# Performance work log

Hardware: AMD Instinct MI355X
Metric: run time of the kernel (lower is better)

## Reference

```python
import math
import jax, jax.numpy as jnp
import numpy as np

B = 65536
EMBED = 256
COND = 256
TIME = 128
HID = 256
E = 8
RHID = 128
IN_DIM = EMBED + TIME + COND  # 640


def setup_inputs() -> dict:
    key = jax.random.key(0)
    ks = jax.random.split(key, 20)
    s = 0.02
    inp = {
        "z_t": jax.random.normal(ks[0], (B, EMBED), jnp.float32),
        "t": jax.random.uniform(ks[1], (B, 1), jnp.float32),
        "cond": jax.random.normal(ks[2], (B, COND), jnp.float32),
        # time embedding proj (Linear(time,time) -> SiLU -> Linear(time,time))
        "tW1": jax.random.normal(ks[3], (TIME, TIME), jnp.float32) * s,
        "tb1": jnp.zeros((TIME,), jnp.float32),
        "tW2": jax.random.normal(ks[4], (TIME, TIME), jnp.float32) * s,
        "tb2": jnp.zeros((TIME,), jnp.float32),
        # stacked expert weights [E, in, out]
        "eW1": jax.random.normal(ks[5], (E, IN_DIM, HID), jnp.float32) * s,
        "eb1": jnp.zeros((E, HID), jnp.float32),
        "eW2": jax.random.normal(ks[6], (E, HID, HID), jnp.float32) * s,
        "eb2": jnp.zeros((E, HID), jnp.float32),
        "eW3": jax.random.normal(ks[7], (E, HID, EMBED), jnp.float32) * s,
        "eb3": jnp.zeros((E, EMBED), jnp.float32),
        # router
        "rW1": jax.random.normal(ks[8], (IN_DIM, RHID), jnp.float32) * s,
        "rb1": jnp.zeros((RHID,), jnp.float32),
        "rW2": jax.random.normal(ks[9], (RHID, E), jnp.float32) * s,
        "rb2": jnp.zeros((E,), jnp.float32),
    }
    return inp


def _time_embedding(t, tW1, tb1, tW2, tb2):
    half = TIME // 2  # 64
    scale = -math.log(10000.0) / (half - 1)
    freqs = jnp.exp(jnp.arange(half, dtype=t.dtype) * scale)[None, :]  # [1, half]
    angles = t * freqs  # [B, half]
    emb = jnp.concatenate([jnp.sin(angles), jnp.cos(angles)], axis=-1)  # [B, TIME]
    h = jax.nn.silu(emb @ tW1 + tb1)
    return h @ tW2 + tb2


def reference(z_t, t, cond, tW1, tb1, tW2, tb2, eW1, eb1, eW2, eb2, eW3, eb3, rW1, rb1, rW2, rb2):
    time_emb = _time_embedding(t, tW1, tb1, tW2, tb2)
    x = jnp.concatenate([z_t, time_emb, cond], axis=-1)  # [B, IN_DIM]
    # dense MoE: all experts via batched GEMMs (dropout=0 -> identity)
    h1 = jax.nn.silu(jnp.einsum('bi,eih->beh', x, eW1) + eb1)      # [B,E,HID]
    h2 = jax.nn.silu(jnp.einsum('beh,ehk->bek', h1, eW2) + eb2)    # [B,E,HID]
    expert_out = jnp.einsum('beh,ehd->bed', h2, eW3) + eb3         # [B,E,EMBED]
    # router softmax gate
    rh = jax.nn.silu(x @ rW1 + rb1)
    gate = jax.nn.softmax(rh @ rW2 + rb2, axis=-1)                 # [B,E]
    velocity = jnp.einsum('be,bed->bd', gate, expert_out)          # [B,EMBED]
    return velocity, gate
```

## Files before the change

### kernel.cpp

```cpp
#include <hip/hip_runtime.h>

typedef __attribute__((ext_vector_type(8))) short bf16x8;
typedef __attribute__((ext_vector_type(4))) float f32x4;

#define NB_ROWS 65536
#define D_EMBED 256
#define D_HID   256
#define N_EXP   8
#define D_RHID  128
#define D_IN    640

#define KSTR 72
#define HSTR 264

static __device__ __forceinline__ ushort f2bf(float f) {
  union { float f; unsigned u; } v; v.f = f;
  unsigned r = v.u + 0x7fffu + ((v.u >> 16) & 1u);
  return (ushort)(r >> 16);
}
static __device__ __forceinline__ float bf2f(ushort h) {
  union { unsigned u; float f; } v; v.u = ((unsigned)h) << 16;
  return v.f;
}
static __device__ __forceinline__ float silu_f(float x) {
  return x / (1.0f + __expf(-x));
}

__global__ void prep_transpose(const float* __restrict__ src, ushort* __restrict__ dst,
                               int R, int C, int total) {
  int idx = blockIdx.x * 256 + threadIdx.x;
  if (idx >= total) return;
  int rc = R * C;
  int m = idx / rc;
  int rem = idx - m * rc;
  int r = rem / C;
  int c = rem - r * C;
  dst[m * rc + c * R + r] = f2bf(src[idx]);
}

static __device__ __forceinline__ void stageA128_512(const ushort* __restrict__ src, int ld,
                                                     int kt, ushort* dst, int tid) {
  uint4 v[2];
  #pragma unroll
  for (int c = 0; c < 2; ++c) {
    int f = c * 8192 + tid * 16;
    int r = f >> 7, ce = (f & 127) >> 1;
    v[c] = *(const uint4*)&src[(size_t)r * ld + kt + ce];
  }
  #pragma unroll
  for (int c = 0; c < 2; ++c) {
    int f = c * 8192 + tid * 16;
    int r = f >> 7, ce = (f & 127) >> 1;
    *(uint4*)&dst[r * KSTR + ce] = v[c];
  }
}
static __device__ __forceinline__ void stageB256_512(const ushort* __restrict__ src, int ld,
                                                     int kt, ushort* dst, int tid) {
  uint4 v[4];
  #pragma unroll
  for (int c = 0; c < 4; ++c) {
    int f = c * 8192 + tid * 16;
    int r = f >> 7, ce = (f & 127) >> 1;
    v[c] = *(const uint4*)&src[(size_t)r * ld + kt + ce];
  }
  #pragma unroll
  for (int c = 0; c < 4; ++c) {
    int f = c * 8192 + tid * 16;
    int r = f >> 7, ce = (f & 127) >> 1;
    *(uint4*)&dst[r * KSTR + ce] = v[c];
  }
}
static __device__ __forceinline__ void stageA128_256(const ushort* __restrict__ src, int ld,
                                                     int kt, ushort* dst, int tid) {
  uint4 v[4];
  #pragma unroll
  for (int c = 0; c < 4; ++c) {
    int f = c * 4096 + tid * 16;
    int r = f >> 7, ce = (f & 127) >> 1;
    v[c] = *(const uint4*)&src[(size_t)r * ld + kt + ce];
  }
  #pragma unroll
  for (int c = 0; c < 4; ++c) {
    int f = c * 4096 + tid * 16;
    int r = f >> 7, ce = (f & 127) >> 1;
    *(uint4*)&dst[r * KSTR + ce] = v[c];
  }
}

__global__ __launch_bounds__(512) void time_x_kernel(
    const float* __restrict__ zt, const float* __restrict__ tin,
    const float* __restrict__ cond,
    const ushort* __restrict__ tw1t, const ushort* __restrict__ tw2t,
    const float* __restrict__ tb1, const float* __restrict__ tb2,
    ushort* __restrict__ x) {
  __shared__ __align__(16) ushort sE[128 * 136];
  __shared__ float sFreq[64];
  __shared__ float sB1[128];
  __shared__ float sB2[128];

  const int tid = threadIdx.x;
  const int row0 = blockIdx.x * 128;

  for (int ch = tid; ch < 128 * 64; ch += 512) {
    int r = ch >> 6;
    int c4 = (ch & 63) << 2;
    size_t grow = (size_t)(row0 + r);
    float4 zv = *(const float4*)&zt[grow * 256 + c4];
    ushort4 o; o.x = f2bf(zv.x); o.y = f2bf(zv.y); o.z = f2bf(zv.z); o.w = f2bf(zv.w);
    *(ushort4*)&x[grow * 640 + c4] = o;
    float4 cv = *(const float4*)&cond[grow * 256 + c4];
    ushort4 o2; o2.x = f2bf(cv.x); o2.y = f2bf(cv.y); o2.z = f2bf(cv.z); o2.w = f2bf(cv.w);
    *(ushort4*)&x[grow * 640 + 384 + c4] = o2;
  }

  if (tid < 64) sFreq[tid] = __expf((float)tid * (-9.210340371976184f / 63.0f));
  if (tid < 128) { sB1[tid] = tb1[tid]; sB2[tid] = tb2[tid]; }
  __syncthreads();

  {
    int r = tid >> 2;
    int qd = tid & 3;
    float tv = tin[row0 + r];
    int half = qd >> 1;
    int cbase = (qd & 1) * 32;
    ushort* er = &sE[r * 136 + half * 64 + cbase];
    #pragma unroll
    for (int c = 0; c < 32; ++c) {
      float a = tv * sFreq[cbase + c];
      float v = half ? __cosf(a) : __sinf(a);
      er[c] = f2bf(v);
    }
  }
  __syncthreads();

  const int l = tid & 63;
  const int w = tid >> 6;
  const int wm = w >> 1;
  const int wn = w & 1;
  const int lr = l & 15;
  const int lk = (l >> 4) * 8;
  const int q4 = (l >> 4) * 4;

  f32x4 acc[2][4] = {};
  #pragma unroll
  for (int kk = 0; kk < 4; ++kk) {
    int kb = kk * 32 + lk;
    bf16x8 av[2], bv[4];
    #pragma unroll
    for (int mf = 0; mf < 2; ++mf)
      av[mf] = *(const bf16x8*)&sE[(wm * 32 + mf * 16 + lr) * 136 + kb];
    #pragma unroll
    for (int nf = 0; nf < 4; ++nf)
      bv[nf] = *(const bf16x8*)&tw1t[(size_t)(wn * 64 + nf * 16 + lr) * 128 + kb];
    #pragma unroll
    for (int mf = 0; mf < 2; ++mf)
      #pragma unroll
      for (int nf = 0; nf < 4; ++nf)
        acc[mf][nf] = __builtin_amdgcn_mfma_f32_16x16x32_bf16(av[mf], bv[nf], acc[mf][nf], 0, 0, 0);
  }
  __syncthreads();
  #pragma unroll
  for (int mf = 0; mf < 2; ++mf)
    #pragma unroll
    for (int nf = 0; nf < 4; ++nf) {
      int cc = wn * 64 + nf * 16 + lr;
      #pragma unroll
      for (int rg = 0; rg < 4; ++rg) {
        int rr = wm * 32 + mf * 16 + q4 + rg;
        sE[rr * 136 + cc] = f2bf(silu_f(acc[mf][nf][rg] + sB1[cc]));
      }
    }
  __syncthreads();

  f32x4 acc2[2][4] = {};
  #pragma unroll
  for (int kk = 0; kk < 4; ++kk) {
    int kb = kk * 32 + lk;
    bf16x8 av[2], bv[4];
    #pragma unroll
    for (int mf = 0; mf < 2; ++mf)
      av[mf] = *(const bf16x8*)&sE[(wm * 32 + mf * 16 + lr) * 136 + kb];
    #pragma unroll
    for (int nf = 0; nf < 4; ++nf)
      bv[nf] = *(const bf16x8*)&tw2t[(size_t)(wn * 64 + nf * 16 + lr) * 128 + kb];
    #pragma unroll
    for (int mf = 0; mf < 2; ++mf)
      #pragma unroll
      for (int nf = 0; nf < 4; ++nf)
        acc2[mf][nf] = __builtin_amdgcn_mfma_f32_16x16x32_bf16(av[mf], bv[nf], acc2[mf][nf], 0, 0, 0);
  }
  #pragma unroll
  for (int mf = 0; mf < 2; ++mf)
    #pragma unroll
    for (int nf = 0; nf < 4; ++nf) {
      int cc = wn * 64 + nf * 16 + lr;
      #pragma unroll
      for (int rg = 0; rg < 4; ++rg) {
        int rr = wm * 32 + mf * 16 + q4 + rg;
        x[(size_t)(row0 + rr) * 640 + 256 + cc] = f2bf(acc2[mf][nf][rg] + sB2[cc]);
      }
    }
}

__global__ __launch_bounds__(256) void router_kernel(
    const ushort* __restrict__ xb, const ushort* __restrict__ rw1t,
    const float* __restrict__ rb1, const float* __restrict__ rW2,
    const float* __restrict__ rb2, float* __restrict__ gatef,
    float* __restrict__ gateo) {
  __shared__ __align__(16) ushort smA[128 * KSTR];
  __shared__ __align__(16) ushort smB[128 * KSTR];
  __shared__ __align__(16) ushort rhbuf[128 * 136];
  __shared__ float sW2[128 * 8];

  const int tid = threadIdx.x;
  const int row0 = blockIdx.x * 128;
  for (int i = tid; i < 1024; i += 256) sW2[i] = rW2[i];

  const int l = tid & 63;
  const int w = tid >> 6;
  const int wm = w >> 1, wn = w & 1;
  const int lr = l & 15, lk = (l >> 4) * 8, q4 = (l >> 4) * 4;
  const ushort* xrow = xb + (size_t)row0 * 640;

  f32x4 acc[4][4] = {};
  for (int kt = 0; kt < 640; kt += 64) {
    stageA128_256(xrow, 640, kt, smA, tid);
    stageA128_256(rw1t, 640, kt, smB, tid);
    __syncthreads();
    #pragma unroll
    for (int kk = 0; kk < 2; ++kk) {
      int kb = kk * 32 + lk;
      bf16x8 av[4], bv[4];
      #pragma unroll
      for (int mf = 0; mf < 4; ++mf)
        av[mf] = *(const bf16x8*)&smA[(wm * 64 + mf * 16 + lr) * KSTR + kb];
      #pragma unroll
      for (int nf = 0; nf < 4; ++nf)
        bv[nf] = *(const bf16x8*)&smB[(wn * 64 + nf * 16 + lr) * KSTR + kb];
      #pragma unroll
      for (int mf = 0; mf < 4; ++mf)
        #pragma unroll
        for (int nf = 0; nf < 4; ++nf)
          acc[mf][nf] = __builtin_amdgcn_mfma_f32_16x16x32_bf16(av[mf], bv[nf], acc[mf][nf], 0, 0, 0);
    }
    __syncthreads();
  }
  #pragma unroll
  for (int nf = 0; nf < 4; ++nf) {
    int cc = wn * 64 + nf * 16 + lr;
    float b1v = rb1[cc];
    #pragma unroll
    for (int mf = 0; mf < 4; ++mf)
      #pragma unroll
      for (int rg = 0; rg < 4; ++rg) {
        int rr = wm * 64 + mf * 16 + q4 + rg;
        rhbuf[rr * 136 + cc] = f2bf(silu_f(acc[mf][nf][rg] + b1v));
      }
  }
  __syncthreads();

  if (tid < 128) {
    float a[8];
    #pragma unroll
    for (int e = 0; e < 8; ++e) a[e] = rb2[e];
    #pragma unroll
    for (int i8 = 0; i8 < 16; ++i8) {
      bf16x8 hv = *(const bf16x8*)&rhbuf[tid * 136 + i8 * 8];
      #pragma unroll
      for (int j = 0; j < 8; ++j) {
        float h = bf2f((ushort)hv[j]);
        const float* wrow = &sW2[(i8 * 8 + j) * 8];
        #pragma unroll
        for (int e = 0; e < 8; ++e) a[e] += h * wrow[e];
      }
    }
    float mx = a[0];
    #pragma unroll
    for (int e = 1; e < 8; ++e) mx = fmaxf(mx, a[e]);
    float s = 0.f, ex[8];
    #pragma unroll
    for (int e = 0; e < 8; ++e) { ex[e] = __expf(a[e] - mx); s += ex[e]; }
    float inv = 1.f / s;
    size_t b = (size_t)(row0 + tid);
    #pragma unroll
    for (int e = 0; e < 8; ++e) {
      float g = ex[e] * inv;
      gatef[b * 8 + e] = g;
      gateo[b * 8 + e] = g;
    }
  }
}

__global__ __launch_bounds__(512) void moe_fused_kernel(
    const ushort* __restrict__ xb, const ushort* __restrict__ w1t,
    const ushort* __restrict__ w2t, const ushort* __restrict__ w3t,
    const float* __restrict__ eb1, const float* __restrict__ eb2,
    const float* __restrict__ eb3, const float* __restrict__ gatef,
    float* __restrict__ velout) {
  __shared__ __align__(16) ushort smA[128 * KSTR];
  __shared__ __align__(16) ushort smB[256 * KSTR];
  __shared__ __align__(16) ushort hbuf[128 * HSTR];
  __shared__ float sGate[128 * 8];
  __shared__ float sEb3[8 * 256];

  const int tid = threadIdx.x;
  const int row0 = blockIdx.x * 128;
  const int l = tid & 63;
  const int w = tid >> 6;
  const int wm = w >> 2;
  const int wn = w & 3;
  const int lr = l & 15;
  const int lk = (l >> 4) * 8;
  const int q4 = (l >> 4) * 4;

  for (int i = tid; i < 1024; i += 512) sGate[i] = gatef[(size_t)row0 * 8 + i];
  for (int i = tid; i < 2048; i += 512) sEb3[i] = eb3[i];

  const ushort* xrow = xb + (size_t)row0 * 640;
  f32x4 vacc[4][4] = {};
  __syncthreads();

  for (int e = 0; e < 8; ++e) {
    const ushort* W1 = w1t + (size_t)e * (256 * 640);
    const ushort* W2 = w2t + (size_t)e * (256 * 256);
    const ushort* W3 = w3t + (size_t)e * (256 * 256);

    f32x4 acc[4][4] = {};
    for (int kt = 0; kt < 640; kt += 64) {
      stageA128_512(xrow, 640, kt, smA, tid);
      stageB256_512(W1, 640, kt, smB, tid);
      __syncthreads();
      #pragma unroll
      for (int kk = 0; kk < 2; ++kk) {
        int kb = kk * 32 + lk;
        bf16x8 av[4], bv[4];
        #pragma unroll
        for (int mf = 0; mf < 4; ++mf)
          av[mf] = *(const bf16x8*)&smA[(wm * 64 + mf * 16 + lr) * KSTR + kb];
        #pragma unroll
        for (int nf = 0; nf < 4; ++nf)
          bv[nf] = *(const bf16x8*)&smB[(wn * 64 + nf * 16 + lr) * KSTR + kb];
        #pragma unroll
        for (int mf = 0; mf < 4; ++mf)
          #pragma unroll
          for (int nf = 0; nf < 4; ++nf)
            acc[mf][nf] = __builtin_amdgcn_mfma_f32_16x16x32_bf16(av[mf], bv[nf], acc[mf][nf], 0, 0, 0);
      }
      __syncthreads();
    }
    #pragma unroll
    for (int nf = 0; nf < 4; ++nf) {
      int cc = wn * 64 + nf * 16 + lr;
      float b1v = eb1[e * 256 + cc];
      #pragma unroll
      for (int mf = 0; mf < 4; ++mf)
        #pragma unroll
        for (int rg = 0; rg < 4; ++rg) {
          int rr = wm * 64 + mf * 16 + q4 + rg;
          hbuf[rr * HSTR + cc] = f2bf(silu_f(acc[mf][nf][rg] + b1v));
        }
    }
    __syncthreads();

    #pragma unroll
    for (int mf = 0; mf < 4; ++mf)
      #pragma unroll
      for (int nf = 0; nf < 4; ++nf)
        acc[mf][nf] = (f32x4){0.f, 0.f, 0.f, 0.f};
    for (int kt = 0; kt < 256; kt += 64) {
      stageB256_512(W2, 256, kt, smB, tid);
      __syncthreads();
      #pragma unroll
      for (int kk = 0; kk < 2; ++kk) {
        int kbl = kk * 32 + lk;
        int kbh = kt + kbl;
        bf16x8 av[4], bv[4];
        #pragma unroll
        for (int mf = 0; mf < 4; ++mf)
          av[mf] = *(const bf16x8*)&hbuf[(wm * 64 + mf * 16 + lr) * HSTR + kbh];
        #pragma unroll
        for (int nf = 0; nf < 4; ++nf)
          bv[nf] = *(const bf16x8*)&smB[(wn * 64 + nf * 16 + lr) * KSTR + kbl];
        #pragma unroll
        for (int mf = 0; mf < 4; ++mf)
          #pragma unroll
          for (int nf = 0; nf < 4; ++nf)
            acc[mf][nf] = __builtin_amdgcn_mfma_f32_16x16x32_bf16(av[mf], bv[nf], acc[mf][nf], 0, 0, 0);
      }
      __syncthreads();
    }
    #pragma unroll
    for (int nf = 0; nf < 4; ++nf) {
      int cc = wn * 64 + nf * 16 + lr;
      float b2v = eb2[e * 256 + cc];
      #pragma unroll
      for (int mf = 0; mf < 4; ++mf)
        #pragma unroll
        for (int rg = 0; rg < 4; ++rg) {
          int rr = wm * 64 + mf * 16 + q4 + rg;
          float gv = sGate[rr * 8 + e];
          hbuf[rr * HSTR + cc] = f2bf(silu_f(acc[mf][nf][rg] + b2v) * gv);
        }
    }
    __syncthreads();

    for (int kt = 0; kt < 256; kt += 64) {
      stageB256_512(W3, 256, kt, smB, tid);
      __syncthreads();
      #pragma unroll
      for (int kk = 0; kk < 2; ++kk) {
        int kbl = kk * 32 + lk;
        int kbh = kt + kbl;
        bf16x8 av[4], bv[4];
        #pragma unroll
        for (int mf = 0; mf < 4; ++mf)
          av[mf] = *(const bf16x8*)&hbuf[(wm * 64 + mf * 16 + lr) * HSTR + kbh];
        #pragma unroll
        for (int nf = 0; nf < 4; ++nf)
          bv[nf] = *(const bf16x8*)&smB[(wn * 64 + nf * 16 + lr) * KSTR + kbl];
        #pragma unroll
        for (int mf = 0; mf < 4; ++mf)
          #pragma unroll
          for (int nf = 0; nf < 4; ++nf)
            vacc[mf][nf] = __builtin_amdgcn_mfma_f32_16x16x32_bf16(av[mf], bv[nf], vacc[mf][nf], 0, 0, 0);
      }
      __syncthreads();
    }
  }

  #pragma unroll
  for (int mf = 0; mf < 4; ++mf)
    #pragma unroll
    for (int rg = 0; rg < 4; ++rg) {
      int rr = wm * 64 + mf * 16 + q4 + rg;
      const float* gp = &sGate[rr * 8];
      #pragma unroll
      for (int nf = 0; nf < 4; ++nf) {
        int cc = wn * 64 + nf * 16 + lr;
        float bsum = 0.f;
        #pragma unroll
        for (int ee = 0; ee < 8; ++ee) bsum += gp[ee] * sEb3[ee * 256 + cc];
        velout[(size_t)(row0 + rr) * D_EMBED + cc] = vacc[mf][nf][rg] + bsum;
      }
    }
}

extern "C" void kernel_launch(void* const* d_in, const int* in_sizes, int n_in,
                              void* d_out, int out_size, void* d_ws, size_t ws_size,
                              hipStream_t stream) {
  const float* zt   = (const float*)d_in[0];
  const float* tin  = (const float*)d_in[1];
  const float* cond = (const float*)d_in[2];
  const float* tW1  = (const float*)d_in[3];
  const float* tb1  = (const float*)d_in[4];
  const float* tW2  = (const float*)d_in[5];
  const float* tb2  = (const float*)d_in[6];
  const float* eW1  = (const float*)d_in[7];
  const float* eb1  = (const float*)d_in[8];
  const float* eW2  = (const float*)d_in[9];
  const float* eb2  = (const float*)d_in[10];
  const float* eW3  = (const float*)d_in[11];
  const float* eb3  = (const float*)d_in[12];
  const float* rW1  = (const float*)d_in[13];
  const float* rb1  = (const float*)d_in[14];
  const float* rW2  = (const float*)d_in[15];
  const float* rb2  = (const float*)d_in[16];

  char* wp = (char*)d_ws;
  ushort* xb    = (ushort*)wp; wp += (size_t)NB_ROWS * D_IN * 2;
  float*  gatef = (float*)wp;  wp += (size_t)NB_ROWS * 8 * 4;
  ushort* w1t   = (ushort*)wp; wp += (size_t)N_EXP * D_HID * D_IN * 2;
  ushort* w2t   = (ushort*)wp; wp += (size_t)N_EXP * D_HID * D_HID * 2;
  ushort* w3t   = (ushort*)wp; wp += (size_t)N_EXP * D_HID * D_EMBED * 2;
  ushort* rw1t  = (ushort*)wp; wp += (size_t)D_RHID * D_IN * 2;
  ushort* tw1t  = (ushort*)wp; wp += (size_t)128 * 128 * 2;
  ushort* tw2t  = (ushort*)wp; wp += (size_t)128 * 128 * 2;

  float* velout  = (float*)d_out;
  float* gateout = velout + (size_t)NB_ROWS * D_EMBED;

  {
    int tot;
    tot = 128 * 128;
    prep_transpose<<<(tot + 255) / 256, 256, 0, stream>>>(tW1, tw1t, 128, 128, tot);
    prep_transpose<<<(tot + 255) / 256, 256, 0, stream>>>(tW2, tw2t, 128, 128, tot);
    tot = D_IN * D_RHID;
    prep_transpose<<<(tot + 255) / 256, 256, 0, stream>>>(rW1, rw1t, D_IN, D_RHID, tot);
    tot = N_EXP * D_IN * D_HID;
    prep_transpose<<<(tot + 255) / 256, 256, 0, stream>>>(eW1, w1t, D_IN, D_HID, tot);
    tot = N_EXP * D_HID * D_HID;
    prep_transpose<<<(tot + 255) / 256, 256, 0, stream>>>(eW2, w2t, D_HID, D_HID, tot);
    tot = N_EXP * D_HID * D_EMBED;
    prep_transpose<<<(tot + 255) / 256, 256, 0, stream>>>(eW3, w3t, D_HID, D_EMBED, tot);
  }

  time_x_kernel<<<512, 512, 0, stream>>>(zt, tin, cond, tw1t, tw2t, tb1, tb2, xb);
  router_kernel<<<512, 256, 0, stream>>>(xb, rw1t, rb1, rW2, rb2, gatef, gateout);
  moe_fused_kernel<<<512, 512, 0, stream>>>(xb, w1t, w2t, w3t, eb1, eb2, eb3, gatef, velout);
}
```

Baseline: 694.2 us.

## Prefetch next K-tile into registers while computing current tile in expert GEMMs

Splits the shared-memory staging helpers into separate global-load and LDS-write steps, so the next K-slice of activations and weights is loaded into registers before the MFMA work on the current slice begins. All three expert GEMM loops now issue their global loads early, which hides load latency behind matrix work. The cost is more live registers, which could lower occupancy in an already register-heavy kernel, and each iteration now has two barriers.

```diff
diff --git a/kernel.cpp b/kernel.cpp
--- a/kernel.cpp
+++ b/kernel.cpp
@@ -38,15 +38,16 @@
   dst[m * rc + c * R + r] = f2bf(src[idx]);
 }
 
-static __device__ __forceinline__ void stageA128_512(const ushort* __restrict__ src, int ld,
-                                                     int kt, ushort* dst, int tid) {
-  uint4 v[2];
+static __device__ __forceinline__ void loadA128_512(const ushort* __restrict__ src, int ld,
+                                                    int kt, int tid, uint4* v) {
   #pragma unroll
   for (int c = 0; c < 2; ++c) {
     int f = c * 8192 + tid * 16;
     int r = f >> 7, ce = (f & 127) >> 1;
     v[c] = *(const uint4*)&src[(size_t)r * ld + kt + ce];
   }
+}
+static __device__ __forceinline__ void writeA128_512(ushort* dst, int tid, const uint4* v) {
   #pragma unroll
   for (int c = 0; c < 2; ++c) {
     int f = c * 8192 + tid * 16;
@@ -54,15 +55,16 @@
     *(uint4*)&dst[r * KSTR + ce] = v[c];
   }
 }
-static __device__ __forceinline__ void stageB256_512(const ushort* __restrict__ src, int ld,
-                                                     int kt, ushort* dst, int tid) {
-  uint4 v[4];
+static __device__ __forceinline__ void loadB256_512(const ushort* __restrict__ src, int ld,
+                                                    int kt, int tid, uint4* v) {
   #pragma unroll
   for (int c = 0; c < 4; ++c) {
     int f = c * 8192 + tid * 16;
     int r = f >> 7, ce = (f & 127) >> 1;
     v[c] = *(const uint4*)&src[(size_t)r * ld + kt + ce];
   }
+}
+static __device__ __forceinline__ void writeB256_512(ushort* dst, int tid, const uint4* v) {
   #pragma unroll
   for (int c = 0; c < 4; ++c) {
     int f = c * 8192 + tid * 16;
@@ -326,27 +328,43 @@
     const ushort* W3 = w3t + (size_t)e * (256 * 256);
 
     f32x4 acc[4][4] = {};
-    for (int kt = 0; kt < 640; kt += 64) {
-      stageA128_512(xrow, 640, kt, smA, tid);
-      stageB256_512(W1, 640, kt, smB, tid);
+    {
+      uint4 va[2], vb[4];
+      loadA128_512(xrow, 640, 0, tid, va);
+      loadB256_512(W1, 640, 0, tid, vb);
+      writeA128_512(smA, tid, va);
+      writeB256_512(smB, tid, vb);
       __syncthreads();
-      #pragma unroll
-      for (int kk = 0; kk < 2; ++kk) {
-        int kb = kk * 32 + lk;
-        bf16x8 av[4], bv[4];
-        #pragma unroll
-        for (int mf = 0; mf < 4; ++mf)
-          av[mf] = *(const bf16x8*)&smA[(wm * 64 + mf * 16 + lr) * KSTR + kb];
-        #pragma unroll
-        for (int nf = 0; nf < 4; ++nf)
-          bv[nf] = *(const bf16x8*)&smB[(wn * 64 + nf * 16 + lr) * KSTR + kb];
-        #pragma unroll
-        for (int mf = 0; mf < 4; ++mf)
+      for (int kt = 0; kt < 640; kt += 64) {
+        const bool more = (kt + 64 < 640);
+        uint4 na[2], nb[4];
+        if (more) {
+          loadA128_512(xrow, 640, kt + 64, tid, na);
+          loadB256_512(W1, 640, kt + 64, tid, nb);
+        }
+        #pragma unroll
+        for (int kk = 0; kk < 2; ++kk) {
+          int kb = kk * 32 + lk;
+          bf16x8 av[4], bv[4];
+          #pragma unroll
+          for (int mf = 0; mf < 4; ++mf)
+            av[mf] = *(const bf16x8*)&smA[(wm * 64 + mf * 16 + lr) * KSTR + kb];
           #pragma unroll
           for (int nf = 0; nf < 4; ++nf)
-            acc[mf][nf] = __builtin_amdgcn_mfma_f32_16x16x32_bf16(av[mf], bv[nf], acc[mf][nf], 0, 0, 0);
-      }
-      __syncthreads();
+            bv[nf] = *(const bf16x8*)&smB[(wn * 64 + nf * 16 + lr) * KSTR + kb];
+          #pragma unroll
+          for (int mf = 0; mf < 4; ++mf)
+            #pragma unroll
+            for (int nf = 0; nf < 4; ++nf)
+              acc[mf][nf] = __builtin_amdgcn_mfma_f32_16x16x32_bf16(av[mf], bv[nf], acc[mf][nf], 0, 0, 0);
+        }
+        __syncthreads();
+        if (more) {
+          writeA128_512(smA, tid, na);
+          writeB256_512(smB, tid, nb);
+        }
+        __syncthreads();
+      }
     }
     #pragma unroll
     for (int nf = 0; nf < 4; ++nf) {
@@ -367,27 +385,36 @@
       #pragma unroll
       for (int nf = 0; nf < 4; ++nf)
         acc[mf][nf] = (f32x4){0.f, 0.f, 0.f, 0.f};
-    for (int kt = 0; kt < 256; kt += 64) {
-      stageB256_512(W2, 256, kt, smB, tid);
+    {
+      uint4 vb[4];
+      loadB256_512(W2, 256, 0, tid, vb);
+      writeB256_512(smB, tid, vb);
       __syncthreads();
-      #pragma unroll
-      for (int kk = 0; kk < 2; ++kk) {
-        int kbl = kk * 32 + lk;
-        int kbh = kt + kbl;
-        bf16x8 av[4], bv[4];
-        #pragma unroll
-        for (int mf = 0; mf < 4; ++mf)
-          av[mf] = *(const bf16x8*)&hbuf[(wm * 64 + mf * 16 + lr) * HSTR + kbh];
-        #pragma unroll
-        for (int nf = 0; nf < 4; ++nf)
-          bv[nf] = *(const bf16x8*)&smB[(wn * 64 + nf * 16 + lr) * KSTR + kbl];
-        #pragma unroll
-        for (int mf = 0; mf < 4; ++mf)
+      for (int kt = 0; kt < 256; kt += 64) {
+        const bool more = (kt + 64 < 256);
+        uint4 nb[4];
+        if (more) loadB256_512(W2, 256, kt + 64, tid, nb);
+        #pragma unroll
+        for (int kk = 0; kk < 2; ++kk) {
+          int kbl = kk * 32 + lk;
+          int kbh = kt + kbl;
+          bf16x8 av[4], bv[4];
+          #pragma unroll
+          for (int mf = 0; mf < 4; ++mf)
+            av[mf] = *(const bf16x8*)&hbuf[(wm * 64 + mf * 16 + lr) * HSTR + kbh];
           #pragma unroll
           for (int nf = 0; nf < 4; ++nf)
-            acc[mf][nf] = __builtin_amdgcn_mfma_f32_16x16x32_bf16(av[mf], bv[nf], acc[mf][nf], 0, 0, 0);
-      }
-      __syncthreads();
+            bv[nf] = *(const bf16x8*)&smB[(wn * 64 + nf * 16 + lr) * KSTR + kbl];
+          #pragma unroll
+          for (int mf = 0; mf < 4; ++mf)
+            #pragma unroll
+            for (int nf = 0; nf < 4; ++nf)
+              acc[mf][nf] = __builtin_amdgcn_mfma_f32_16x16x32_bf16(av[mf], bv[nf], acc[mf][nf], 0, 0, 0);
+        }
+        __syncthreads();
+        if (more) writeB256_512(smB, tid, nb);
+        __syncthreads();
+      }
     }
     #pragma unroll
     for (int nf = 0; nf < 4; ++nf) {
@@ -404,27 +431,36 @@
     }
     __syncthreads();
 
-    for (int kt = 0; kt < 256; kt += 64) {
-      stageB256_512(W3, 256, kt, smB, tid);
+    {
+      uint4 vb[4];
+      loadB256_512(W3, 256, 0, tid, vb);
+      writeB256_512(smB, tid, vb);
       __syncthreads();
-      #pragma unroll
-      for (int kk = 0; kk < 2; ++kk) {
-        int kbl = kk * 32 + lk;
-        int kbh = kt + kbl;
-        bf16x8 av[4], bv[4];
-        #pragma unroll
-        for (int mf = 0; mf < 4; ++mf)
-          av[mf] = *(const bf16x8*)&hbuf[(wm * 64 + mf * 16 + lr) * HSTR + kbh];
-        #pragma unroll
-        for (int nf = 0; nf < 4; ++nf)
-          bv[nf] = *(const bf16x8*)&smB[(wn * 64 + nf * 16 + lr) * KSTR + kbl];
-        #pragma unroll
-        for (int mf = 0; mf < 4; ++mf)
+      for (int kt = 0; kt < 256; kt += 64) {
+        const bool more = (kt + 64 < 256);
+        uint4 nb[4];
+        if (more) loadB256_512(W3, 256, kt + 64, tid, nb);
+        #pragma unroll
+        for (int kk = 0; kk < 2; ++kk) {
+          int kbl = kk * 32 + lk;
+          int kbh = kt + kbl;
+          bf16x8 av[4], bv[4];
+          #pragma unroll
+          for (int mf = 0; mf < 4; ++mf)
+            av[mf] = *(const bf16x8*)&hbuf[(wm * 64 + mf * 16 + lr) * HSTR + kbh];
           #pragma unroll
           for (int nf = 0; nf < 4; ++nf)
-            vacc[mf][nf] = __builtin_amdgcn_mfma_f32_16x16x32_bf16(av[mf], bv[nf], vacc[mf][nf], 0, 0, 0);
-      }
-      __syncthreads();
+            bv[nf] = *(const bf16x8*)&smB[(wn * 64 + nf * 16 + lr) * KSTR + kbl];
+          #pragma unroll
+          for (int mf = 0; mf < 4; ++mf)
+            #pragma unroll
+            for (int nf = 0; nf < 4; ++nf)
+              vacc[mf][nf] = __builtin_amdgcn_mfma_f32_16x16x32_bf16(av[mf], bv[nf], vacc[mf][nf], 0, 0, 0);
+        }
+        __syncthreads();
+        if (more) writeB256_512(smB, tid, nb);
+        __syncthreads();
+      }
     }
   }
 
```

After: 1.032 ms. +48.7%, slower.

## Halve MoE row tile, swizzle hidden buffer, and double grid for occupancy

Applied to the files above, without the earlier changes.

The fused MoE kernel now handles 64 rows per block instead of 128 and launches 1024 blocks. Per-wave accumulators shrink to 2x4 fragments and the launch bounds ask for several resident blocks. The padded hidden buffer becomes an XOR-swizzled 64x256 layout to avoid LDS bank conflicts without padding. The expert-3 bias table is loaded into the reused A-staging buffer only at the end, so LDS drops enough for more blocks per CU, giving better latency hiding. In exchange, expert weight tiles are re-staged twice as often per row, and the tighter register budget risks spills.

```diff
diff --git a/kernel.cpp b/kernel.cpp
--- a/kernel.cpp
+++ b/kernel.cpp
@@ -11,7 +11,6 @@
 #define D_IN    640
 
 #define KSTR 72
-#define HSTR 264
 
 static __device__ __forceinline__ ushort f2bf(float f) {
   union { float f; unsigned u; } v; v.f = f;
@@ -24,6 +23,10 @@
 }
 static __device__ __forceinline__ float silu_f(float x) {
   return x / (1.0f + __expf(-x));
+}
+
+static __device__ __forceinline__ int hswz(int r, int c) {
+  return r * 256 + ((((c) >> 3) ^ (r & 7)) << 3) + ((c) & 7);
 }
 
 __global__ void prep_transpose(const float* __restrict__ src, ushort* __restrict__ dst,
@@ -38,21 +41,12 @@
   dst[m * rc + c * R + r] = f2bf(src[idx]);
 }
 
-static __device__ __forceinline__ void stageA128_512(const ushort* __restrict__ src, int ld,
-                                                     int kt, ushort* dst, int tid) {
-  uint4 v[2];
-  #pragma unroll
-  for (int c = 0; c < 2; ++c) {
-    int f = c * 8192 + tid * 16;
-    int r = f >> 7, ce = (f & 127) >> 1;
-    v[c] = *(const uint4*)&src[(size_t)r * ld + kt + ce];
-  }
-  #pragma unroll
-  for (int c = 0; c < 2; ++c) {
-    int f = c * 8192 + tid * 16;
-    int r = f >> 7, ce = (f & 127) >> 1;
-    *(uint4*)&dst[r * KSTR + ce] = v[c];
-  }
+static __device__ __forceinline__ void stageA64_512(const ushort* __restrict__ src, int ld,
+                                                    int kt, ushort* dst, int tid) {
+  int f = tid * 16;
+  int r = f >> 7, ce = (f & 127) >> 1;
+  uint4 v = *(const uint4*)&src[(size_t)r * ld + kt + ce];
+  *(uint4*)&dst[r * KSTR + ce] = v;
 }
 static __device__ __forceinline__ void stageB256_512(const ushort* __restrict__ src, int ld,
                                                      int kt, ushort* dst, int tid) {
@@ -291,20 +285,19 @@
   }
 }
 
-__global__ __launch_bounds__(512) void moe_fused_kernel(
+__global__ __launch_bounds__(512, 4) void moe_fused_kernel(
     const ushort* __restrict__ xb, const ushort* __restrict__ w1t,
     const ushort* __restrict__ w2t, const ushort* __restrict__ w3t,
     const float* __restrict__ eb1, const float* __restrict__ eb2,
     const float* __restrict__ eb3, const float* __restrict__ gatef,
     float* __restrict__ velout) {
-  __shared__ __align__(16) ushort smA[128 * KSTR];
+  __shared__ __align__(16) ushort smA[64 * KSTR];
   __shared__ __align__(16) ushort smB[256 * KSTR];
-  __shared__ __align__(16) ushort hbuf[128 * HSTR];
-  __shared__ float sGate[128 * 8];
-  __shared__ float sEb3[8 * 256];
+  __shared__ __align__(16) ushort hbuf[64 * 256];
+  __shared__ float sGate[64 * 8];
 
   const int tid = threadIdx.x;
-  const int row0 = blockIdx.x * 128;
+  const int row0 = blockIdx.x * 64;
   const int l = tid & 63;
   const int w = tid >> 6;
   const int wm = w >> 2;
@@ -313,11 +306,10 @@
   const int lk = (l >> 4) * 8;
   const int q4 = (l >> 4) * 4;
 
-  for (int i = tid; i < 1024; i += 512) sGate[i] = gatef[(size_t)row0 * 8 + i];
-  for (int i = tid; i < 2048; i += 512) sEb3[i] = eb3[i];
+  for (int i = tid; i < 512; i += 512) sGate[i] = gatef[(size_t)row0 * 8 + i];
 
   const ushort* xrow = xb + (size_t)row0 * 640;
-  f32x4 vacc[4][4] = {};
+  f32x4 vacc[2][4] = {};
   __syncthreads();
 
   for (int e = 0; e < 8; ++e) {
@@ -325,23 +317,23 @@
     const ushort* W2 = w2t + (size_t)e * (256 * 256);
     const ushort* W3 = w3t + (size_t)e * (256 * 256);
 
-    f32x4 acc[4][4] = {};
+    f32x4 acc[2][4] = {};
     for (int kt = 0; kt < 640; kt += 64) {
-      stageA128_512(xrow, 640, kt, smA, tid);
+      stageA64_512(xrow, 640, kt, smA, tid);
       stageB256_512(W1, 640, kt, smB, tid);
       __syncthreads();
       #pragma unroll
       for (int kk = 0; kk < 2; ++kk) {
         int kb = kk * 32 + lk;
-        bf16x8 av[4], bv[4];
-        #pragma unroll
-        for (int mf = 0; mf < 4; ++mf)
-          av[mf] = *(const bf16x8*)&smA[(wm * 64 + mf * 16 + lr) * KSTR + kb];
+        bf16x8 av[2], bv[4];
+        #pragma unroll
+        for (int mf = 0; mf < 2; ++mf)
+          av[mf] = *(const bf16x8*)&smA[(wm * 32 + mf * 16 + lr) * KSTR + kb];
         #pragma unroll
         for (int nf = 0; nf < 4; ++nf)
           bv[nf] = *(const bf16x8*)&smB[(wn * 64 + nf * 16 + lr) * KSTR + kb];
         #pragma unroll
-        for (int mf = 0; mf < 4; ++mf)
+        for (int mf = 0; mf < 2; ++mf)
           #pragma unroll
           for (int nf = 0; nf < 4; ++nf)
             acc[mf][nf] = __builtin_amdgcn_mfma_f32_16x16x32_bf16(av[mf], bv[nf], acc[mf][nf], 0, 0, 0);
@@ -353,17 +345,17 @@
       int cc = wn * 64 + nf * 16 + lr;
       float b1v = eb1[e * 256 + cc];
       #pragma unroll
-      for (int mf = 0; mf < 4; ++mf)
+      for (int mf = 0; mf < 2; ++mf)
         #pragma unroll
         for (int rg = 0; rg < 4; ++rg) {
-          int rr = wm * 64 + mf * 16 + q4 + rg;
-          hbuf[rr * HSTR + cc] = f2bf(silu_f(acc[mf][nf][rg] + b1v));
+          int rr = wm * 32 + mf * 16 + q4 + rg;
+          hbuf[hswz(rr, cc)] = f2bf(silu_f(acc[mf][nf][rg] + b1v));
         }
     }
     __syncthreads();
 
     #pragma unroll
-    for (int mf = 0; mf < 4; ++mf)
+    for (int mf = 0; mf < 2; ++mf)
       #pragma unroll
       for (int nf = 0; nf < 4; ++nf)
         acc[mf][nf] = (f32x4){0.f, 0.f, 0.f, 0.f};
@@ -374,15 +366,15 @@
       for (int kk = 0; kk < 2; ++kk) {
         int kbl = kk * 32 + lk;
         int kbh = kt + kbl;
-        bf16x8 av[4], bv[4];
-        #pragma unroll
-        for (int mf = 0; mf < 4; ++mf)
-          av[mf] = *(const bf16x8*)&hbuf[(wm * 64 + mf * 16 + lr) * HSTR + kbh];
+        bf16x8 av[2], bv[4];
+        #pragma unroll
+        for (int mf = 0; mf < 2; ++mf)
+          av[mf] = *(const bf16x8*)&hbuf[hswz(wm * 32 + mf * 16 + lr, kbh)];
         #pragma unroll
         for (int nf = 0; nf < 4; ++nf)
           bv[nf] = *(const bf16x8*)&smB[(wn * 64 + nf * 16 + lr) * KSTR + kbl];
         #pragma unroll
-        for (int mf = 0; mf < 4; ++mf)
+        for (int mf = 0; mf < 2; ++mf)
           #pragma unroll
           for (int nf = 0; nf < 4; ++nf)
             acc[mf][nf] = __builtin_amdgcn_mfma_f32_16x16x32_bf16(av[mf], bv[nf], acc[mf][nf], 0, 0, 0);
@@ -394,12 +386,12 @@
       int cc = wn * 64 + nf * 16 + lr;
       float b2v = eb2[e * 256 + cc];
       #pragma unroll
-      for (int mf = 0; mf < 4; ++mf)
+      for (int mf = 0; mf < 2; ++mf)
         #pragma unroll
         for (int rg = 0; rg < 4; ++rg) {
-          int rr = wm * 64 + mf * 16 + q4 + rg;
+          int rr = wm * 32 + mf * 16 + q4 + rg;
           float gv = sGate[rr * 8 + e];
-          hbuf[rr * HSTR + cc] = f2bf(silu_f(acc[mf][nf][rg] + b2v) * gv);
+          hbuf[hswz(rr, cc)] = f2bf(silu_f(acc[mf][nf][rg] + b2v) * gv);
         }
     }
     __syncthreads();
@@ -411,15 +403,15 @@
       for (int kk = 0; kk < 2; ++kk) {
         int kbl = kk * 32 + lk;
         int kbh = kt + kbl;
-        bf16x8 av[4], bv[4];
-        #pragma unroll
-        for (int mf = 0; mf < 4; ++mf)
-          av[mf] = *(const bf16x8*)&hbuf[(wm * 64 + mf * 16 + lr) * HSTR + kbh];
+        bf16x8 av[2], bv[4];
+        #pragma unroll
+        for (int mf = 0; mf < 2; ++mf)
+          av[mf] = *(const bf16x8*)&hbuf[hswz(wm * 32 + mf * 16 + lr, kbh)];
         #pragma unroll
         for (int nf = 0; nf < 4; ++nf)
           bv[nf] = *(const bf16x8*)&smB[(wn * 64 + nf * 16 + lr) * KSTR + kbl];
         #pragma unroll
-        for (int mf = 0; mf < 4; ++mf)
+        for (int mf = 0; mf < 2; ++mf)
           #pragma unroll
           for (int nf = 0; nf < 4; ++nf)
             vacc[mf][nf] = __builtin_amdgcn_mfma_f32_16x16x32_bf16(av[mf], bv[nf], vacc[mf][nf], 0, 0, 0);
@@ -428,18 +420,21 @@
     }
   }
 
-  #pragma unroll
-  for (int mf = 0; mf < 4; ++mf)
+  float* eL = (float*)smA;
+  for (int i = tid; i < 2048; i += 512) eL[i] = eb3[i];
+  __syncthreads();
+  #pragma unroll
+  for (int mf = 0; mf < 2; ++mf)
     #pragma unroll
     for (int rg = 0; rg < 4; ++rg) {
-      int rr = wm * 64 + mf * 16 + q4 + rg;
+      int rr = wm * 32 + mf * 16 + q4 + rg;
       const float* gp = &sGate[rr * 8];
       #pragma unroll
       for (int nf = 0; nf < 4; ++nf) {
         int cc = wn * 64 + nf * 16 + lr;
         float bsum = 0.f;
         #pragma unroll
-        for (int ee = 0; ee < 8; ++ee) bsum += gp[ee] * sEb3[ee * 256 + cc];
+        for (int ee = 0; ee < 8; ++ee) bsum += gp[ee] * eL[ee * 256 + cc];
         velout[(size_t)(row0 + rr) * D_EMBED + cc] = vacc[mf][nf][rg] + bsum;
       }
     }
@@ -496,5 +491,5 @@
 
   time_x_kernel<<<512, 512, 0, stream>>>(zt, tin, cond, tw1t, tw2t, tb1, tb2, xb);
   router_kernel<<<512, 256, 0, stream>>>(xb, rw1t, rb1, rW2, rb2, gatef, gateout);
-  moe_fused_kernel<<<512, 512, 0, stream>>>(xb, w1t, w2t, w3t, eb1, eb2, eb3, gatef, velout);
-}
+  moe_fused_kernel<<<1024, 512, 0, stream>>>(xb, w1t, w2t, w3t, eb1, eb2, eb3, gatef, velout);
+}
```

New measurement: 1.100 ms. 58.4% more time.

## Stream expert weights from global directly into MFMA, keep x tile resident

Applied to the files above, without the earlier changes.

The fused MoE kernel now loads the block's 64x640 input tile into LDS once, and each wave reads its slice of the expert weight columns straight from global/L2 into registers for MFMA. This removes per-k-tile weight staging through LDS and most barriers. The row tile is halved to 64 with 1024 blocks, and the final bias table reuses the x buffer. In exchange, each block re-reads all expert weights from global with less reuse per load, and the directly loaded operands have no LDS-based latency hiding.

```diff
diff --git a/kernel.cpp b/kernel.cpp
--- a/kernel.cpp
+++ b/kernel.cpp
@@ -11,6 +11,7 @@
 #define D_IN    640
 
 #define KSTR 72
+#define XSTR 648
 #define HSTR 264
 
 static __device__ __forceinline__ ushort f2bf(float f) {
@@ -38,38 +39,6 @@
   dst[m * rc + c * R + r] = f2bf(src[idx]);
 }
 
-static __device__ __forceinline__ void stageA128_512(const ushort* __restrict__ src, int ld,
-                                                     int kt, ushort* dst, int tid) {
-  uint4 v[2];
-  #pragma unroll
-  for (int c = 0; c < 2; ++c) {
-    int f = c * 8192 + tid * 16;
-    int r = f >> 7, ce = (f & 127) >> 1;
-    v[c] = *(const uint4*)&src[(size_t)r * ld + kt + ce];
-  }
-  #pragma unroll
-  for (int c = 0; c < 2; ++c) {
-    int f = c * 8192 + tid * 16;
-    int r = f >> 7, ce = (f & 127) >> 1;
-    *(uint4*)&dst[r * KSTR + ce] = v[c];
-  }
-}
-static __device__ __forceinline__ void stageB256_512(const ushort* __restrict__ src, int ld,
-                                                     int kt, ushort* dst, int tid) {
-  uint4 v[4];
-  #pragma unroll
-  for (int c = 0; c < 4; ++c) {
-    int f = c * 8192 + tid * 16;
-    int r = f >> 7, ce = (f & 127) >> 1;
-    v[c] = *(const uint4*)&src[(size_t)r * ld + kt + ce];
-  }
-  #pragma unroll
-  for (int c = 0; c < 4; ++c) {
-    int f = c * 8192 + tid * 16;
-    int r = f >> 7, ce = (f & 127) >> 1;
-    *(uint4*)&dst[r * KSTR + ce] = v[c];
-  }
-}
 static __device__ __forceinline__ void stageA128_256(const ushort* __restrict__ src, int ld,
                                                      int kt, ushort* dst, int tid) {
   uint4 v[4];
@@ -291,155 +260,150 @@
   }
 }
 
-__global__ __launch_bounds__(512) void moe_fused_kernel(
+__global__ __launch_bounds__(512) void moe_stream_kernel(
     const ushort* __restrict__ xb, const ushort* __restrict__ w1t,
     const ushort* __restrict__ w2t, const ushort* __restrict__ w3t,
     const float* __restrict__ eb1, const float* __restrict__ eb2,
     const float* __restrict__ eb3, const float* __restrict__ gatef,
     float* __restrict__ velout) {
-  __shared__ __align__(16) ushort smA[128 * KSTR];
-  __shared__ __align__(16) ushort smB[256 * KSTR];
-  __shared__ __align__(16) ushort hbuf[128 * HSTR];
-  __shared__ float sGate[128 * 8];
-  __shared__ float sEb3[8 * 256];
+  __shared__ __align__(16) ushort xbuf[64 * XSTR];
+  __shared__ __align__(16) ushort hbuf[64 * HSTR];
+  __shared__ float sGate[64 * 8];
 
   const int tid = threadIdx.x;
-  const int row0 = blockIdx.x * 128;
+  const int row0 = blockIdx.x * 64;
   const int l = tid & 63;
   const int w = tid >> 6;
-  const int wm = w >> 2;
-  const int wn = w & 3;
   const int lr = l & 15;
   const int lk = (l >> 4) * 8;
   const int q4 = (l >> 4) * 4;
 
-  for (int i = tid; i < 1024; i += 512) sGate[i] = gatef[(size_t)row0 * 8 + i];
-  for (int i = tid; i < 2048; i += 512) sEb3[i] = eb3[i];
-
-  const ushort* xrow = xb + (size_t)row0 * 640;
-  f32x4 vacc[4][4] = {};
-  __syncthreads();
+  {
+    const ushort* xrow = xb + (size_t)row0 * 640;
+    #pragma unroll
+    for (int c = 0; c < 10; ++c) {
+      int f = c * 8192 + tid * 16;
+      int r = f / 1280;
+      int ce = (f - r * 1280) >> 1;
+      *(uint4*)&xbuf[r * XSTR + ce] = *(const uint4*)&xrow[(size_t)r * 640 + ce];
+    }
+  }
+  if (tid < 512) sGate[tid] = gatef[(size_t)row0 * 8 + tid];
+  __syncthreads();
+
+  f32x4 vacc[4][2] = {};
 
   for (int e = 0; e < 8; ++e) {
     const ushort* W1 = w1t + (size_t)e * (256 * 640);
     const ushort* W2 = w2t + (size_t)e * (256 * 256);
     const ushort* W3 = w3t + (size_t)e * (256 * 256);
-
-    f32x4 acc[4][4] = {};
-    for (int kt = 0; kt < 640; kt += 64) {
-      stageA128_512(xrow, 640, kt, smA, tid);
-      stageB256_512(W1, 640, kt, smB, tid);
-      __syncthreads();
-      #pragma unroll
-      for (int kk = 0; kk < 2; ++kk) {
-        int kb = kk * 32 + lk;
-        bf16x8 av[4], bv[4];
-        #pragma unroll
-        for (int mf = 0; mf < 4; ++mf)
-          av[mf] = *(const bf16x8*)&smA[(wm * 64 + mf * 16 + lr) * KSTR + kb];
-        #pragma unroll
-        for (int nf = 0; nf < 4; ++nf)
-          bv[nf] = *(const bf16x8*)&smB[(wn * 64 + nf * 16 + lr) * KSTR + kb];
-        #pragma unroll
-        for (int mf = 0; mf < 4; ++mf)
-          #pragma unroll
-          for (int nf = 0; nf < 4; ++nf)
-            acc[mf][nf] = __builtin_amdgcn_mfma_f32_16x16x32_bf16(av[mf], bv[nf], acc[mf][nf], 0, 0, 0);
-      }
-      __syncthreads();
-    }
-    #pragma unroll
-    for (int nf = 0; nf < 4; ++nf) {
-      int cc = wn * 64 + nf * 16 + lr;
+    const ushort* b1p0 = W1 + (size_t)(w * 32 + lr) * 640;
+    const ushort* b1p1 = W1 + (size_t)(w * 32 + 16 + lr) * 640;
+
+    f32x4 acc[4][2] = {};
+    #pragma unroll 4
+    for (int ks = 0; ks < 20; ++ks) {
+      int kb = ks * 32 + lk;
+      bf16x8 av[4], bv[2];
+      bv[0] = *(const bf16x8*)&b1p0[kb];
+      bv[1] = *(const bf16x8*)&b1p1[kb];
+      #pragma unroll
+      for (int mf = 0; mf < 4; ++mf)
+        av[mf] = *(const bf16x8*)&xbuf[(mf * 16 + lr) * XSTR + kb];
+      #pragma unroll
+      for (int mf = 0; mf < 4; ++mf)
+        #pragma unroll
+        for (int nf = 0; nf < 2; ++nf)
+          acc[mf][nf] = __builtin_amdgcn_mfma_f32_16x16x32_bf16(av[mf], bv[nf], acc[mf][nf], 0, 0, 0);
+    }
+    __syncthreads();
+    #pragma unroll
+    for (int nf = 0; nf < 2; ++nf) {
+      int cc = w * 32 + nf * 16 + lr;
       float b1v = eb1[e * 256 + cc];
       #pragma unroll
       for (int mf = 0; mf < 4; ++mf)
         #pragma unroll
         for (int rg = 0; rg < 4; ++rg) {
-          int rr = wm * 64 + mf * 16 + q4 + rg;
+          int rr = mf * 16 + q4 + rg;
           hbuf[rr * HSTR + cc] = f2bf(silu_f(acc[mf][nf][rg] + b1v));
         }
     }
     __syncthreads();
 
+    const ushort* b2p0 = W2 + (size_t)(w * 32 + lr) * 256;
+    const ushort* b2p1 = W2 + (size_t)(w * 32 + 16 + lr) * 256;
     #pragma unroll
     for (int mf = 0; mf < 4; ++mf)
       #pragma unroll
-      for (int nf = 0; nf < 4; ++nf)
+      for (int nf = 0; nf < 2; ++nf)
         acc[mf][nf] = (f32x4){0.f, 0.f, 0.f, 0.f};
-    for (int kt = 0; kt < 256; kt += 64) {
-      stageB256_512(W2, 256, kt, smB, tid);
-      __syncthreads();
-      #pragma unroll
-      for (int kk = 0; kk < 2; ++kk) {
-        int kbl = kk * 32 + lk;
-        int kbh = kt + kbl;
-        bf16x8 av[4], bv[4];
-        #pragma unroll
-        for (int mf = 0; mf < 4; ++mf)
-          av[mf] = *(const bf16x8*)&hbuf[(wm * 64 + mf * 16 + lr) * HSTR + kbh];
-        #pragma unroll
-        for (int nf = 0; nf < 4; ++nf)
-          bv[nf] = *(const bf16x8*)&smB[(wn * 64 + nf * 16 + lr) * KSTR + kbl];
-        #pragma unroll
-        for (int mf = 0; mf < 4; ++mf)
-          #pragma unroll
-          for (int nf = 0; nf < 4; ++nf)
-            acc[mf][nf] = __builtin_amdgcn_mfma_f32_16x16x32_bf16(av[mf], bv[nf], acc[mf][nf], 0, 0, 0);
-      }
-      __syncthreads();
-    }
-    #pragma unroll
-    for (int nf = 0; nf < 4; ++nf) {
-      int cc = wn * 64 + nf * 16 + lr;
+    #pragma unroll 4
+    for (int ks = 0; ks < 8; ++ks) {
+      int kb = ks * 32 + lk;
+      bf16x8 av[4], bv[2];
+      bv[0] = *(const bf16x8*)&b2p0[kb];
+      bv[1] = *(const bf16x8*)&b2p1[kb];
+      #pragma unroll
+      for (int mf = 0; mf < 4; ++mf)
+        av[mf] = *(const bf16x8*)&hbuf[(mf * 16 + lr) * HSTR + kb];
+      #pragma unroll
+      for (int mf = 0; mf < 4; ++mf)
+        #pragma unroll
+        for (int nf = 0; nf < 2; ++nf)
+          acc[mf][nf] = __builtin_amdgcn_mfma_f32_16x16x32_bf16(av[mf], bv[nf], acc[mf][nf], 0, 0, 0);
+    }
+    __syncthreads();
+    #pragma unroll
+    for (int nf = 0; nf < 2; ++nf) {
+      int cc = w * 32 + nf * 16 + lr;
       float b2v = eb2[e * 256 + cc];
       #pragma unroll
       for (int mf = 0; mf < 4; ++mf)
         #pragma unroll
         for (int rg = 0; rg < 4; ++rg) {
-          int rr = wm * 64 + mf * 16 + q4 + rg;
+          int rr = mf * 16 + q4 + rg;
           float gv = sGate[rr * 8 + e];
           hbuf[rr * HSTR + cc] = f2bf(silu_f(acc[mf][nf][rg] + b2v) * gv);
         }
     }
     __syncthreads();
 
-    for (int kt = 0; kt < 256; kt += 64) {
-      stageB256_512(W3, 256, kt, smB, tid);
-      __syncthreads();
-      #pragma unroll
-      for (int kk = 0; kk < 2; ++kk) {
-        int kbl = kk * 32 + lk;
-        int kbh = kt + kbl;
-        bf16x8 av[4], bv[4];
-        #pragma unroll
-        for (int mf = 0; mf < 4; ++mf)
-          av[mf] = *(const bf16x8*)&hbuf[(wm * 64 + mf * 16 + lr) * HSTR + kbh];
-        #pragma unroll
-        for (int nf = 0; nf < 4; ++nf)
-          bv[nf] = *(const bf16x8*)&smB[(wn * 64 + nf * 16 + lr) * KSTR + kbl];
-        #pragma unroll
-        for (int mf = 0; mf < 4; ++mf)
-          #pragma unroll
-          for (int nf = 0; nf < 4; ++nf)
-            vacc[mf][nf] = __builtin_amdgcn_mfma_f32_16x16x32_bf16(av[mf], bv[nf], vacc[mf][nf], 0, 0, 0);
-      }
-      __syncthreads();
-    }
-  }
-
+    const ushort* b3p0 = W3 + (size_t)(w * 32 + lr) * 256;
+    const ushort* b3p1 = W3 + (size_t)(w * 32 + 16 + lr) * 256;
+    #pragma unroll 4
+    for (int ks = 0; ks < 8; ++ks) {
+      int kb = ks * 32 + lk;
+      bf16x8 av[4], bv[2];
+      bv[0] = *(const bf16x8*)&b3p0[kb];
+      bv[1] = *(const bf16x8*)&b3p1[kb];
+      #pragma unroll
+      for (int mf = 0; mf < 4; ++mf)
+        av[mf] = *(const bf16x8*)&hbuf[(mf * 16 + lr) * HSTR + kb];
+      #pragma unroll
+      for (int mf = 0; mf < 4; ++mf)
+        #pragma unroll
+        for (int nf = 0; nf < 2; ++nf)
+          vacc[mf][nf] = __builtin_amdgcn_mfma_f32_16x16x32_bf16(av[mf], bv[nf], vacc[mf][nf], 0, 0, 0);
+    }
+  }
+
+  __syncthreads();
+  float* eL = (float*)xbuf;
+  for (int i = tid; i < 2048; i += 512) eL[i] = eb3[i];
+  __syncthreads();
   #pragma unroll
   for (int mf = 0; mf < 4; ++mf)
     #pragma unroll
     for (int rg = 0; rg < 4; ++rg) {
-      int rr = wm * 64 + mf * 16 + q4 + rg;
+      int rr = mf * 16 + q4 + rg;
       const float* gp = &sGate[rr * 8];
       #pragma unroll
-      for (int nf = 0; nf < 4; ++nf) {
-        int cc = wn * 64 + nf * 16 + lr;
+      for (int nf = 0; nf < 2; ++nf) {
+        int cc = w * 32 + nf * 16 + lr;
         float bsum = 0.f;
         #pragma unroll
-        for (int ee = 0; ee < 8; ++ee) bsum += gp[ee] * sEb3[ee * 256 + cc];
+        for (int ee = 0; ee < 8; ++ee) bsum += gp[ee] * eL[ee * 256 + cc];
         velout[(size_t)(row0 + rr) * D_EMBED + cc] = vacc[mf][nf][rg] + bsum;
       }
     }
@@ -496,5 +460,6 @@
 
   time_x_kernel<<<512, 512, 0, stream>>>(zt, tin, cond, tw1t, tw2t, tb1, tb2, xb);
   router_kernel<<<512, 256, 0, stream>>>(xb, rw1t, rb1, rW2, rb2, gatef, gateout);
-  moe_fused_kernel<<<512, 512, 0, stream>>>(xb, w1t, w2t, w3t, eb1, eb2, eb3, gatef, velout);
-}
+  moe_stream_kernel<<<1024, 512, 0, stream>>>(xb, w1t, w2t, w3t,
+                                              eb1, eb2, eb3, gatef, velout);
+}
```

Result: slower. 834.2 us (+20.2%).
